# Optimization experiments

Measured on AMD Instinct MI355X. Metric: run time of the kernel, lower is better.

## Reference

```python
import jax, jax.numpy as jnp
import numpy as np

B, L, D_MODEL, N_HEADS = 2, 2048, 1024, 16
HEAD_DIM = D_MODEL // N_HEADS  # 64
PAD_START = (3 * L) // 4  # last quarter of keys are padding


def _rope_tables(seq_len, dim, base=10000.0, dtype=jnp.float32):
    inv_freq = 1.0 / (base ** (jnp.arange(0, dim, 2, dtype=jnp.float32) / dim))
    t = jnp.arange(seq_len, dtype=jnp.float32)
    freqs = jnp.einsum('i,j->ij', t, inv_freq)  # (L, dim/2)
    return jnp.cos(freqs).astype(dtype), jnp.sin(freqs).astype(dtype)


def _apply_rope(x, cos, sin):
    # x: (B, H, L, D); cos/sin: (L, D/2)
    cos = cos[None, None]
    sin = sin[None, None]
    x_even, x_odd = x[..., 0::2], x[..., 1::2]
    rot_even = x_even * cos - x_odd * sin
    rot_odd = x_even * sin + x_odd * cos
    return jnp.stack((rot_even, rot_odd), axis=-1).reshape(x.shape)


def setup_inputs() -> dict:
    key = jax.random.key(0)
    k_x, k_wqkv, k_bqkv, k_wout, k_bout = jax.random.split(key, 5)
    x = jax.random.normal(k_x, (B, L, D_MODEL), dtype=jnp.float32)
    Wqkv = jax.random.normal(k_wqkv, (3 * D_MODEL, D_MODEL), dtype=jnp.float32) * 0.02
    bqkv = jax.random.normal(k_bqkv, (3 * D_MODEL,), dtype=jnp.float32) * 0.02
    Wout = jax.random.normal(k_wout, (D_MODEL, D_MODEL), dtype=jnp.float32) * 0.02
    bout = jax.random.normal(k_bout, (D_MODEL,), dtype=jnp.float32) * 0.02
    # True = padded position (end of sequence padded)
    pad_mask = jnp.broadcast_to(jnp.arange(L) >= PAD_START, (B, L))
    return {"x": x, "pad_mask": pad_mask, "Wqkv": Wqkv, "bqkv": bqkv, "Wout": Wout, "bout": bout}


def reference(x, pad_mask, Wqkv, bqkv, Wout, bout):
    Bc, Lc, E = x.shape
    H, D = N_HEADS, HEAD_DIM
    qkv = x @ Wqkv.T + bqkv                       # (B, L, 3E)
    qkv = qkv.reshape(Bc, Lc, 3, H, D)
    q = jnp.transpose(qkv[:, :, 0], (0, 2, 1, 3))  # (B, H, L, D)
    k = jnp.transpose(qkv[:, :, 1], (0, 2, 1, 3))
    v = jnp.transpose(qkv[:, :, 2], (0, 2, 1, 3))
    cos, sin = _rope_tables(Lc, D, dtype=x.dtype)
    q = _apply_rope(q, cos, sin)
    k = _apply_rope(k, cos, sin)
    # Mask exactly as the torch module builds it: attn_mask = causal_upper | key_pad,
    # with torch bool-mask semantics (True = allowed to attend).
    causal_upper = jnp.triu(jnp.ones((Lc, Lc), dtype=bool), 1)[None, None]  # (1,1,L,L)
    key_pad = pad_mask[:, None, None, :]                                     # (B,1,1,L)
    allowed = causal_upper | key_pad                                         # (B,1,L,L)
    scale = 1.0 / jnp.sqrt(jnp.asarray(D, dtype=x.dtype))
    scores = jnp.einsum('bhqd,bhkd->bhqk', q, k) * scale
    scores = jnp.where(allowed, scores, -jnp.inf)
    attn = jax.nn.softmax(scores, axis=-1)
    out = jnp.einsum('bhqk,bhkd->bhqd', attn, v)   # (B, H, L, D)
    out = jnp.transpose(out, (0, 2, 1, 3)).reshape(Bc, Lc, E)
    return out @ Wout.T + bout
```

## Files before the change

kernel.cpp:

```cpp
#include <hip/hip_runtime.h>

#define BB 2
#define LL 2048
#define DM 1024
#define NH 16
#define HD 64
#define PAD_START 1536

typedef short bf16x8 __attribute__((ext_vector_type(8)));
typedef float f32x4 __attribute__((ext_vector_type(4)));

#define MFMA_B16(a, b, c) __builtin_amdgcn_mfma_f32_16x16x32_bf16(a, b, c, 0, 0, 0)

#define GLOAD_LDS16(g, l)                                            \
    __builtin_amdgcn_global_load_lds(                                \
        (const __attribute__((address_space(1))) void*)(g),          \
        (__attribute__((address_space(3))) void*)(l), 16, 0, 0)

__device__ __forceinline__ float bf2f(unsigned short u) {
    union { unsigned int i; float f; } v; v.i = ((unsigned int)u) << 16; return v.f;
}
__device__ __forceinline__ unsigned short f2bf(float f) {
    union { float f; unsigned int i; } v; v.f = f;
    unsigned int x = v.i;
    return (unsigned short)((x + 0x7fffu + ((x >> 16) & 1u)) >> 16);
}

__global__ __launch_bounds__(256) void split_kernel(
    const float* __restrict__ X, const float* __restrict__ Wq,
    const float* __restrict__ Wo,
    unsigned short* __restrict__ Xh,
    unsigned short* __restrict__ Wh,
    unsigned short* __restrict__ Woh,
    float* __restrict__ cosT, float* __restrict__ sinT)
{
    if (blockIdx.x >= 8192) {
        const int idx = (blockIdx.x - 8192) * 256 + threadIdx.x;
        const int l = idx >> 5, pp = idx & 31;
        const float LOG2_1E4 = 13.287712379549449f;
        const float invf = exp2f(-((float)pp) * (LOG2_1E4 / 32.0f));
        const float ang = (float)l * invf;
        float2 cs; cs.x = cosf(ang); cs.y = sinf(ang);
        ((float2*)cosT)[idx] = cs;
        return;
    }
    const size_t e = ((size_t)blockIdx.x * 256 + threadIdx.x) * 4;
    const float* src; unsigned short* dh; size_t o;
    if (e < 4194304)      { src = X;  dh = Xh;  o = e; }
    else if (e < 7340032) { src = Wq; dh = Wh;  o = e - 4194304; }
    else                  { src = Wo; dh = Woh; o = e - 7340032; }
    float4 v = *(const float4*)(src + o);
    ushort4 hv;
    hv.x = f2bf(v.x); hv.y = f2bf(v.y);
    hv.z = f2bf(v.z); hv.w = f2bf(v.w);
    *(ushort4*)(dh + o) = hv;
}

__device__ __forceinline__ void qk_frag(
    f32x4 cf, int r0, int bh, int d, float bv, float qscale,
    const float2* __restrict__ ct2,
    unsigned short* __restrict__ dst, bool odd)
{
    const int p = d >> 1;
#pragma unroll
    for (int e = 0; e < 4; ++e) {
        const int l = (r0 + e) & (LL - 1);
        const float x = cf[e] + bv;
        const float px = __shfl_xor(x, 1);
        const float2 cs = ct2[l * 32 + p];
        const float ve = odd ? px : x;
        const float vo = odd ? x : px;
        float res = odd ? (ve * cs.y + vo * cs.x) : (ve * cs.x - vo * cs.y);
        res *= qscale;
        const float other = __shfl_xor(res, 1);
        if (!odd) {
            const unsigned int pk = ((unsigned int)f2bf(res)) |
                                    (((unsigned int)f2bf(other)) << 16);
            *(unsigned int*)(dst + ((size_t)bh * LL + l) * HD + d) = pk;
        }
    }
}

__device__ __forceinline__ void v_frag(
    f32x4 cf, int l0, int bh, int d, float bv, unsigned short* __restrict__ vt)
{
    ushort4 pk;
    pk.x = f2bf(cf[0] + bv); pk.y = f2bf(cf[1] + bv);
    pk.z = f2bf(cf[2] + bv); pk.w = f2bf(cf[3] + bv);
    *(ushort4*)(vt + ((size_t)(bh * HD + d)) * LL + l0) = pk;
}

__device__ __forceinline__ void out_frag(
    f32x4 cf, int r0, int c, float bv, float* __restrict__ C)
{
#pragma unroll
    for (int e = 0; e < 4; ++e)
        C[(size_t)(r0 + e) * DM + c] = cf[e] + bv;
}

__global__ __launch_bounds__(512) void qkv_mfma(
    const unsigned short* __restrict__ Xh,
    const unsigned short* __restrict__ Wh,
    const float* __restrict__ bias,
    const float* __restrict__ cosT,
    unsigned short* __restrict__ qs, unsigned short* __restrict__ ks,
    unsigned short* __restrict__ vt)
{
    __shared__ unsigned short As[2 * 256 * 64];
    __shared__ unsigned short Bs[2 * 192 * 64];

    const int bid = blockIdx.y * 16 + blockIdx.x;
    const int xcd = bid & 7;
    const int i   = bid >> 3;
    const int mt  = (xcd & 3) * 4 + (i & 3);
    const int nt  = (xcd >> 2) * 8 + (i >> 2);
    const int m0 = mt * 256, n0 = nt * 192;

    const int t = threadIdx.x;
    const int lane = t & 63;
    const int w = t >> 6;
    const int wm = w >> 2;
    const int wn = w & 3;
    const int lm = lane & 15;
    const int quad = lane >> 4;

    const int rop = lane >> 3;
    const int sw  = ((lane & 7) ^ rop) * 8;
    const unsigned short* ga = Xh + (size_t)(m0 + w * 32 + rop) * 1024 + sw;
    const unsigned short* gb = Wh + (size_t)(n0 + w * 24 + rop) * 1024 + sw;
    unsigned short* lA = As + (w * 32) * 64;
    unsigned short* lB = Bs + (w * 24) * 64;

    const int o1 = (quad ^ (lm & 7)) * 8;
    const int o2 = ((quad + 4) ^ (lm & 7)) * 8;
    const int ar = (wm * 128 + lm) * 64;
    const int br = (wn * 48 + lm) * 64;

    f32x4 acc[8][3];
#pragma unroll
    for (int mf = 0; mf < 8; ++mf)
#pragma unroll
        for (int nf = 0; nf < 3; ++nf) acc[mf][nf] = (f32x4){0.f,0.f,0.f,0.f};

#define STG(ABO, BBO, k0)                                                 \
    do {                                                                  \
        GLOAD_LDS16(ga + (k0),             lA + (ABO));                   \
        GLOAD_LDS16(ga + (k0) +  8 * 1024, lA + (ABO) +  8 * 64);         \
        GLOAD_LDS16(ga + (k0) + 16 * 1024, lA + (ABO) + 16 * 64);         \
        GLOAD_LDS16(ga + (k0) + 24 * 1024, lA + (ABO) + 24 * 64);         \
        GLOAD_LDS16(gb + (k0),             lB + (BBO));                   \
        GLOAD_LDS16(gb + (k0) +  8 * 1024, lB + (BBO) +  8 * 64);         \
        GLOAD_LDS16(gb + (k0) + 16 * 1024, lB + (BBO) + 16 * 64);         \
    } while (0)

#define TILE(ABO, BBO, SG, KS, VMN)                                      \
    {                                                                     \
        bf16x8 af[8][2]; bf16x8 bfr[3][2];                                \
        _Pragma("unroll")                                                 \
        for (int mf = 0; mf < 8; ++mf) {                                  \
            af[mf][0] = *(const bf16x8*)(As + (ABO) + ar + mf * 1024 + o1);\
            af[mf][1] = *(const bf16x8*)(As + (ABO) + ar + mf * 1024 + o2);\
        }                                                                 \
        _Pragma("unroll")                                                 \
        for (int nf = 0; nf < 3; ++nf) {                                  \
            bfr[nf][0] = *(const bf16x8*)(Bs + (BBO) + br + nf * 1024 + o1);\
            bfr[nf][1] = *(const bf16x8*)(Bs + (BBO) + br + nf * 1024 + o2);\
        }                                                                 \
        asm volatile("s_waitcnt lgkmcnt(0)" ::: "memory");                \
        __builtin_amdgcn_sched_barrier(0);                                \
        __builtin_amdgcn_s_barrier();                                     \
        if (SG) { STG(ABO, BBO, KS); }      \
        asm volatile("s_waitcnt vmcnt(" VMN ")" ::: "memory");            \
        __builtin_amdgcn_sched_barrier(0);                                \
        __builtin_amdgcn_s_barrier();                                     \
        __builtin_amdgcn_s_setprio(1);                                    \
        _Pragma("unroll")                                                 \
        for (int mf = 0; mf < 8; ++mf) {                                  \
            _Pragma("unroll")                                             \
            for (int nf = 0; nf < 3; ++nf) {                              \
                acc[mf][nf] = MFMA_B16(af[mf][0], bfr[nf][0], acc[mf][nf]);\
                acc[mf][nf] = MFMA_B16(af[mf][1], bfr[nf][1], acc[mf][nf]);\
            }                                                             \
        }                                                                 \
        __builtin_amdgcn_s_setprio(0);                                    \
    }

    STG(0, 0, 0);
    STG(16384, 12288, 64);
    asm volatile("s_waitcnt vmcnt(7)" ::: "memory");
    __builtin_amdgcn_sched_barrier(0);
    __builtin_amdgcn_s_barrier();

    for (int k0 = 0; k0 < 896; k0 += 128) {
        TILE(0,     0,     1, k0 + 128, "7")
        TILE(16384, 12288, 1, k0 + 192, "7")
    }
    TILE(0,     0,     0, 0, "0")
    TILE(16384, 12288, 0, 0, "0")
#undef TILE
#undef STG

    const int bi = m0 >> 11;
    const int rbase = m0 + wm * 128;
    const int cbase = n0 + wn * 48;
    const bool odd = (lm & 1) != 0;
    const float2* ct2 = (const float2*)cosT;

#pragma unroll
    for (int nf = 0; nf < 3; ++nf) {
        const int col0 = cbase + nf * 16;
        const int s = col0 >> 10;
        const int h = (col0 & 1023) >> 6;
        const int bh = bi * NH + h;
        const int d = (col0 & 63) + lm;
        const float bv = bias[col0 + lm];
        if (s == 2) {
#pragma unroll
            for (int mf = 0; mf < 8; ++mf)
                v_frag(acc[mf][nf], (rbase + mf * 16 + quad * 4) & (LL - 1),
                       bh, d, bv, vt);
        } else {
            unsigned short* dst = (s == 0) ? qs : ks;
            const float qscale = (s == 0) ? 0.125f : 1.0f;
#pragma unroll
            for (int mf = 0; mf < 8; ++mf)
                qk_frag(acc[mf][nf], rbase + mf * 16 + quad * 4, bh,
                        d, bv, qscale, ct2, dst, odd);
        }
    }
}

__global__ __launch_bounds__(256) void attn_mfma(
    const unsigned short* __restrict__ qs,
    const unsigned short* __restrict__ ks,
    const unsigned short* __restrict__ vt,
    unsigned short* __restrict__ aoh)
{
    __shared__ unsigned short Ks[2][64 * 64];
    __shared__ unsigned short Vs[2][64 * 64];
    __shared__ unsigned short Pl[8][16 * 72];

    const int bid = blockIdx.y * 16 + blockIdx.x;
    const int xcd = bid & 7;
    const int j   = bid >> 3;
    const int bh  = xcd * 4 + (j & 3);
    const int qp  = j >> 2;
    const int qtA = qp;
    const int qtB = 31 - qp;
    const int q0A = qtA * 64, q0B = qtB * 64;
    const int b = bh >> 4, h = bh & (NH - 1);
    const int tid = threadIdx.x;
    const int w = tid >> 6;
    const int lane = tid & 63;
    const int lm = lane & 15;
    const int quad = lane >> 4;
    const int qwA = q0A + w * 16;
    const int qwB = q0B + w * 16;

    const unsigned short* qbA = qs + ((size_t)bh * LL + qwA + lm) * HD + quad * 8;
    const unsigned short* qbB = qs + ((size_t)bh * LL + qwB + lm) * HD + quad * 8;
    const bf16x8 qfA0 = *(const bf16x8*)(qbA);
    const bf16x8 qfA1 = *(const bf16x8*)(qbA + 32);
    const bf16x8 qfB0 = *(const bf16x8*)(qbB);
    const bf16x8 qfB1 = *(const bf16x8*)(qbB + 32);

    f32x4 OA[4], OB[4];
#pragma unroll
    for (int dd = 0; dd < 4; ++dd) {
        OA[dd] = (f32x4){0.f, 0.f, 0.f, 0.f};
        OB[dd] = (f32x4){0.f, 0.f, 0.f, 0.f};
    }
    float lrA[4] = {0.f, 0.f, 0.f, 0.f};
    float lrB[4] = {0.f, 0.f, 0.f, 0.f};

    const unsigned short* kbase = ks + (size_t)bh * LL * HD;
    const unsigned short* vtb   = vt + (size_t)bh * HD * LL;
    unsigned short* pwA = &Pl[w][0];
    unsigned short* pwB = &Pl[w + 4][0];

    const int rop = lane >> 3;
    const int sw8 = ((lane & 7) ^ rop) * 8;
    const int r0 = w * 16 + rop;
    const int r1 = w * 16 + 8 + rop;
    const int o1 = (quad ^ (lm & 7)) * 8;
    const int o2 = ((quad + 4) ^ (lm & 7)) * 8;

#define ASTAGE(BUF, KK)                                                      \
    do {                                                                     \
        GLOAD_LDS16(kbase + (size_t)((KK) + r0) * HD + sw8,                  \
                    &Ks[BUF][0] + (w * 2) * 512);                            \
        GLOAD_LDS16(kbase + (size_t)((KK) + r1) * HD + sw8,                  \
                    &Ks[BUF][0] + (w * 2 + 1) * 512);                        \
        GLOAD_LDS16(vtb + (size_t)r0 * LL + (KK) + sw8,                      \
                    &Vs[BUF][0] + (w * 2) * 512);                            \
        GLOAD_LDS16(vtb + (size_t)r1 * LL + (KK) + sw8,                      \
                    &Vs[BUF][0] + (w * 2 + 1) * 512);                        \
    } while (0)

    const int t0A = qtA;
    const int t0B = (qtB < 24) ? qtB : 24;

    ASTAGE(t0A & 1, t0A * 64);
    __syncthreads();

    for (int tt = t0A; tt < 32; ++tt) {
        const int k0 = tt * 64;
        const int cur = tt & 1;
        const unsigned short* Kc = &Ks[cur][0];
        const unsigned short* Vc = &Vs[cur][0];
        const bool doB = (tt >= t0B);

        {
            const int kn = ((tt + 1) < 32 ? (tt + 1) : 31) * 64;
            ASTAGE(cur ^ 1, kn);
        }

        f32x4 sfA[4], sfB[4];
#pragma unroll
        for (int c = 0; c < 4; ++c) {
            const bf16x8 kf0 = *(const bf16x8*)(Kc + (c * 16 + lm) * 64 + o1);
            const bf16x8 kf1 = *(const bf16x8*)(Kc + (c * 16 + lm) * 64 + o2);
            f32x4 zA = (f32x4){0.f, 0.f, 0.f, 0.f};
            zA = MFMA_B16(qfA0, kf0, zA);
            zA = MFMA_B16(qfA1, kf1, zA);
            sfA[c] = zA;
            f32x4 zB = (f32x4){0.f, 0.f, 0.f, 0.f};
            if (doB) {
                zB = MFMA_B16(qfB0, kf0, zB);
                zB = MFMA_B16(qfB1, kf1, zB);
            }
            sfB[c] = zB;
        }
        if (tt == t0A) {
#pragma unroll
            for (int c = 0; c < 4; ++c) {
                const int kg = k0 + c * 16 + lm;
#pragma unroll
                for (int r = 0; r < 4; ++r) {
                    if (kg <= qwA + quad * 4 + r) sfA[c][r] = -1e30f;
                }
            }
        }
        if (doB && tt == t0B && qtB < 24) {
#pragma unroll
            for (int c = 0; c < 4; ++c) {
                const int kg = k0 + c * 16 + lm;
#pragma unroll
                for (int r = 0; r < 4; ++r) {
                    if (kg <= qwB + quad * 4 + r) sfB[c][r] = -1e30f;
                }
            }
        }

#pragma unroll
        for (int r = 0; r < 4; ++r) {
#pragma unroll
            for (int c = 0; c < 4; ++c) {
                const float pA = __expf(sfA[c][r]);
                lrA[r] += pA;
                pwA[(quad * 4 + r) * 72 + c * 16 + lm] = f2bf(pA);
            }
        }
        if (doB) {
#pragma unroll
            for (int r = 0; r < 4; ++r) {
#pragma unroll
                for (int c = 0; c < 4; ++c) {
                    const float pB = __expf(sfB[c][r]);
                    lrB[r] += pB;
                    pwB[(quad * 4 + r) * 72 + c * 16 + lm] = f2bf(pB);
                }
            }
        }

        const bf16x8 aA0 = *(const bf16x8*)(pwA + lm * 72 + quad * 8);
        const bf16x8 aA1 = *(const bf16x8*)(pwA + lm * 72 + 32 + quad * 8);
#pragma unroll
        for (int dd = 0; dd < 4; ++dd) {
            const bf16x8 b0 = *(const bf16x8*)(Vc + (dd * 16 + lm) * 64 + o1);
            const bf16x8 b1 = *(const bf16x8*)(Vc + (dd * 16 + lm) * 64 + o2);
            OA[dd] = MFMA_B16(aA0, b0, OA[dd]);
            OA[dd] = MFMA_B16(aA1, b1, OA[dd]);
        }
        if (doB) {
            const bf16x8 aB0 = *(const bf16x8*)(pwB + lm * 72 + quad * 8);
            const bf16x8 aB1 = *(const bf16x8*)(pwB + lm * 72 + 32 + quad * 8);
#pragma unroll
            for (int dd = 0; dd < 4; ++dd) {
                const bf16x8 b0 = *(const bf16x8*)(Vc + (dd * 16 + lm) * 64 + o1);
                const bf16x8 b1 = *(const bf16x8*)(Vc + (dd * 16 + lm) * 64 + o2);
                OB[dd] = MFMA_B16(aB0, b0, OB[dd]);
                OB[dd] = MFMA_B16(aB1, b1, OB[dd]);
            }
        }

        __syncthreads();
    }
#undef ASTAGE

#pragma unroll
    for (int r = 0; r < 4; ++r) {
        float rsA = lrA[r];
        rsA += __shfl_xor(rsA, 1);
        rsA += __shfl_xor(rsA, 2);
        rsA += __shfl_xor(rsA, 4);
        rsA += __shfl_xor(rsA, 8);
        lrA[r] = rsA;
        float rsB = lrB[r];
        rsB += __shfl_xor(rsB, 1);
        rsB += __shfl_xor(rsB, 2);
        rsB += __shfl_xor(rsB, 4);
        rsB += __shfl_xor(rsB, 8);
        lrB[r] = rsB;
    }

#pragma unroll
    for (int r = 0; r < 4; ++r) {
        const float invA = 1.0f / lrA[r];
        const int qgA = qwA + quad * 4 + r;
        const size_t baseA = ((size_t)(b * LL + qgA)) * DM + h * HD;
#pragma unroll
        for (int dd = 0; dd < 4; ++dd)
            aoh[baseA + dd * 16 + lm] = f2bf(OA[dd][r] * invA);
        const float invB = 1.0f / lrB[r];
        const int qgB = qwB + quad * 4 + r;
        const size_t baseB = ((size_t)(b * LL + qgB)) * DM + h * HD;
#pragma unroll
        for (int dd = 0; dd < 4; ++dd)
            aoh[baseB + dd * 16 + lm] = f2bf(OB[dd][r] * invB);
    }
}

__global__ __launch_bounds__(256) void out_mfma(
    const unsigned short* __restrict__ Ah,
    const unsigned short* __restrict__ Wh,
    const float* __restrict__ bias, float* __restrict__ C)
{
    __shared__ unsigned short As[128 * 64];
    __shared__ unsigned short Bs[128 * 64];
    const int n0 = blockIdx.x * 128;
    const int m0 = blockIdx.y * 128;

    f32x4 c00 = {0,0,0,0}, c01 = {0,0,0,0}, c02 = {0,0,0,0}, c03 = {0,0,0,0};
    f32x4 c10 = {0,0,0,0}, c11 = {0,0,0,0}, c12 = {0,0,0,0}, c13 = {0,0,0,0};
    f32x4 c20 = {0,0,0,0}, c21 = {0,0,0,0}, c22 = {0,0,0,0}, c23 = {0,0,0,0};
    f32x4 c30 = {0,0,0,0}, c31 = {0,0,0,0}, c32 = {0,0,0,0}, c33 = {0,0,0,0};

    const int t = threadIdx.x;
    const int lane = t & 63;
    const int w = t >> 6;
    const int wm = (w >> 1) << 6;
    const int wn = (w & 1) << 6;
    const int lm = lane & 15;
    const int quad = lane >> 4;

    const int rop = lane >> 3;
    const int sw  = ((lane & 7) ^ rop) * 8;
    const unsigned short* ga = Ah + (size_t)(m0 + w * 32 + rop) * 1024 + sw;
    const unsigned short* gb = Wh + (size_t)(n0 + w * 32 + rop) * 1024 + sw;
    unsigned short* lA = As + (w * 32) * 64;
    unsigned short* lB = Bs + (w * 32) * 64;

    const int o1 = (quad ^ (lm & 7)) * 8;
    const int o2 = ((quad + 4) ^ (lm & 7)) * 8;
    const int arow = (wm + lm) * 64;
    const int brow = (wn + lm) * 64;

    for (int k0 = 0; k0 < 1024; k0 += 64) {
        __syncthreads();
        GLOAD_LDS16(ga + k0,             lA);
        GLOAD_LDS16(ga + k0 +  8 * 1024, lA +  8 * 64);
        GLOAD_LDS16(ga + k0 + 16 * 1024, lA + 16 * 64);
        GLOAD_LDS16(ga + k0 + 24 * 1024, lA + 24 * 64);
        GLOAD_LDS16(gb + k0,             lB);
        GLOAD_LDS16(gb + k0 +  8 * 1024, lB +  8 * 64);
        GLOAD_LDS16(gb + k0 + 16 * 1024, lB + 16 * 64);
        GLOAD_LDS16(gb + k0 + 24 * 1024, lB + 24 * 64);
        __syncthreads();
        {
            bf16x8 a0 = *(const bf16x8*)(As + arow +  0 * 64 + o1);
            bf16x8 a1 = *(const bf16x8*)(As + arow + 16 * 64 + o1);
            bf16x8 a2 = *(const bf16x8*)(As + arow + 32 * 64 + o1);
            bf16x8 a3 = *(const bf16x8*)(As + arow + 48 * 64 + o1);
            bf16x8 b0 = *(const bf16x8*)(Bs + brow +  0 * 64 + o1);
            bf16x8 b1 = *(const bf16x8*)(Bs + brow + 16 * 64 + o1);
            bf16x8 b2 = *(const bf16x8*)(Bs + brow + 32 * 64 + o1);
            bf16x8 b3 = *(const bf16x8*)(Bs + brow + 48 * 64 + o1);
            c00 = MFMA_B16(a0, b0, c00); c01 = MFMA_B16(a0, b1, c01);
            c02 = MFMA_B16(a0, b2, c02); c03 = MFMA_B16(a0, b3, c03);
            c10 = MFMA_B16(a1, b0, c10); c11 = MFMA_B16(a1, b1, c11);
            c12 = MFMA_B16(a1, b2, c12); c13 = MFMA_B16(a1, b3, c13);
            c20 = MFMA_B16(a2, b0, c20); c21 = MFMA_B16(a2, b1, c21);
            c22 = MFMA_B16(a2, b2, c22); c23 = MFMA_B16(a2, b3, c23);
            c30 = MFMA_B16(a3, b0, c30); c31 = MFMA_B16(a3, b1, c31);
            c32 = MFMA_B16(a3, b2, c32); c33 = MFMA_B16(a3, b3, c33);
        }
        {
            bf16x8 a0 = *(const bf16x8*)(As + arow +  0 * 64 + o2);
            bf16x8 a1 = *(const bf16x8*)(As + arow + 16 * 64 + o2);
            bf16x8 a2 = *(const bf16x8*)(As + arow + 32 * 64 + o2);
            bf16x8 a3 = *(const bf16x8*)(As + arow + 48 * 64 + o2);
            bf16x8 b0 = *(const bf16x8*)(Bs + brow +  0 * 64 + o2);
            bf16x8 b1 = *(const bf16x8*)(Bs + brow + 16 * 64 + o2);
            bf16x8 b2 = *(const bf16x8*)(Bs + brow + 32 * 64 + o2);
            bf16x8 b3 = *(const bf16x8*)(Bs + brow + 48 * 64 + o2);
            c00 = MFMA_B16(a0, b0, c00); c01 = MFMA_B16(a0, b1, c01);
            c02 = MFMA_B16(a0, b2, c02); c03 = MFMA_B16(a0, b3, c03);
            c10 = MFMA_B16(a1, b0, c10); c11 = MFMA_B16(a1, b1, c11);
            c12 = MFMA_B16(a1, b2, c12); c13 = MFMA_B16(a1, b3, c13);
            c20 = MFMA_B16(a2, b0, c20); c21 = MFMA_B16(a2, b1, c21);
            c22 = MFMA_B16(a2, b2, c22); c23 = MFMA_B16(a2, b3, c23);
            c30 = MFMA_B16(a3, b0, c30); c31 = MFMA_B16(a3, b1, c31);
            c32 = MFMA_B16(a3, b2, c32); c33 = MFMA_B16(a3, b3, c33);
        }
    }

#define CSTORE(rt, ct) \
    out_frag(c##rt##ct, m0 + wm + rt * 16 + quad * 4, \
             n0 + wn + ct * 16 + lm, bias[n0 + wn + ct * 16 + lm], C);
    CSTORE(0,0) CSTORE(0,1) CSTORE(0,2) CSTORE(0,3)
    CSTORE(1,0) CSTORE(1,1) CSTORE(1,2) CSTORE(1,3)
    CSTORE(2,0) CSTORE(2,1) CSTORE(2,2) CSTORE(2,3)
    CSTORE(3,0) CSTORE(3,1) CSTORE(3,2) CSTORE(3,3)
#undef CSTORE
}

extern "C" void kernel_launch(void* const* d_in, const int* in_sizes, int n_in,
                              void* d_out, int out_size, void* d_ws, size_t ws_size,
                              hipStream_t stream)
{
    const float* x    = (const float*)d_in[0];
    const float* Wqkv = (const float*)d_in[2];
    const float* bqkv = (const float*)d_in[3];
    const float* Wout = (const float*)d_in[4];
    const float* bout = (const float*)d_in[5];
    float* out = (float*)d_out;

    unsigned short* p = (unsigned short*)d_ws;
    const size_t SZ = (size_t)BB * NH * LL * HD;
    unsigned short* qsb = p; p += SZ;
    unsigned short* ksb = p; p += SZ;
    unsigned short* vtb = p; p += SZ;
    unsigned short* Xhi = p; p += SZ;
    unsigned short* Whi = p; p += (size_t)3145728;
    unsigned short* Wohi = p; p += (size_t)1048576;
    float* cosT = (float*)p; p += (size_t)4 * 65536;

    split_kernel<<<8448, 256, 0, stream>>>(x, Wqkv, Wout,
                                           Xhi, Whi, Wohi, cosT, nullptr);
    dim3 g1(16, 16);
    qkv_mfma<<<g1, 512, 0, stream>>>(Xhi, Whi, bqkv, cosT,
                                     qsb, ksb, vtb);
    dim3 g2(16, 32);
    attn_mfma<<<g2, 256, 0, stream>>>(qsb, ksb, vtb, Xhi);
    dim3 g3(8, 32);
    out_mfma<<<g3, 256, 0, stream>>>(Xhi, Wohi, bout, out);
}
```

Measured before the change: 200.1 us.

## Double-buffer out-projection GEMM, simplify RoPE epilogue, drop sched barriers and setprio

The output-projection GEMM now uses two LDS buffers, so the next 64-wide K slice is loaded while the current one feeds the MFMAs. This removes the load-then-compute serialisation and one barrier per step, at the cost of twice the LDS. The QKV RoPE epilogue now lets even lanes compute both rotated outputs directly, which removes one shuffle and the odd-lane cos/sin load. The sched_barrier and setprio hints in the QKV GEMM main loop are also removed, which hands instruction ordering back to the compiler.

```diff
diff --git a/kernel.cpp b/kernel.cpp
--- a/kernel.cpp
+++ b/kernel.cpp
@@ -59,23 +59,20 @@
 __device__ __forceinline__ void qk_frag(
     f32x4 cf, int r0, int bh, int d, float bv, float qscale,
     const float2* __restrict__ ct2,
-    unsigned short* __restrict__ dst, bool odd)
+    unsigned short* __restrict__ dst, bool even)
 {
     const int p = d >> 1;
 #pragma unroll
     for (int e = 0; e < 4; ++e) {
         const int l = (r0 + e) & (LL - 1);
         const float x = cf[e] + bv;
-        const float px = __shfl_xor(x, 1);
-        const float2 cs = ct2[l * 32 + p];
-        const float ve = odd ? px : x;
-        const float vo = odd ? x : px;
-        float res = odd ? (ve * cs.y + vo * cs.x) : (ve * cs.x - vo * cs.y);
-        res *= qscale;
-        const float other = __shfl_xor(res, 1);
-        if (!odd) {
-            const unsigned int pk = ((unsigned int)f2bf(res)) |
-                                    (((unsigned int)f2bf(other)) << 16);
+        const float xo = __shfl_xor(x, 1);
+        if (even) {
+            const float2 cs = ct2[l * 32 + p];
+            const float re = (x * cs.x - xo * cs.y) * qscale;
+            const float ro = (x * cs.y + xo * cs.x) * qscale;
+            const unsigned int pk = ((unsigned int)f2bf(re)) |
+                                    (((unsigned int)f2bf(ro)) << 16);
             *(unsigned int*)(dst + ((size_t)bh * LL + l) * HD + d) = pk;
         }
     }
@@ -167,13 +164,10 @@
             bfr[nf][1] = *(const bf16x8*)(Bs + (BBO) + br + nf * 1024 + o2);\
         }                                                                 \
         asm volatile("s_waitcnt lgkmcnt(0)" ::: "memory");                \
-        __builtin_amdgcn_sched_barrier(0);                                \
         __builtin_amdgcn_s_barrier();                                     \
         if (SG) { STG(ABO, BBO, KS); }      \
         asm volatile("s_waitcnt vmcnt(" VMN ")" ::: "memory");            \
-        __builtin_amdgcn_sched_barrier(0);                                \
         __builtin_amdgcn_s_barrier();                                     \
-        __builtin_amdgcn_s_setprio(1);                                    \
         _Pragma("unroll")                                                 \
         for (int mf = 0; mf < 8; ++mf) {                                  \
             _Pragma("unroll")                                             \
@@ -182,13 +176,11 @@
                 acc[mf][nf] = MFMA_B16(af[mf][1], bfr[nf][1], acc[mf][nf]);\
             }                                                             \
         }                                                                 \
-        __builtin_amdgcn_s_setprio(0);                                    \
     }
 
     STG(0, 0, 0);
     STG(16384, 12288, 64);
     asm volatile("s_waitcnt vmcnt(7)" ::: "memory");
-    __builtin_amdgcn_sched_barrier(0);
     __builtin_amdgcn_s_barrier();
 
     for (int k0 = 0; k0 < 896; k0 += 128) {
@@ -203,7 +195,7 @@
     const int bi = m0 >> 11;
     const int rbase = m0 + wm * 128;
     const int cbase = n0 + wn * 48;
-    const bool odd = (lm & 1) != 0;
+    const bool even = (lm & 1) == 0;
     const float2* ct2 = (const float2*)cosT;
 
 #pragma unroll
@@ -225,7 +217,7 @@
 #pragma unroll
             for (int mf = 0; mf < 8; ++mf)
                 qk_frag(acc[mf][nf], rbase + mf * 16 + quad * 4, bh,
-                        d, bv, qscale, ct2, dst, odd);
+                        d, bv, qscale, ct2, dst, even);
         }
     }
 }
@@ -436,8 +428,8 @@
     const unsigned short* __restrict__ Wh,
     const float* __restrict__ bias, float* __restrict__ C)
 {
-    __shared__ unsigned short As[128 * 64];
-    __shared__ unsigned short Bs[128 * 64];
+    __shared__ unsigned short As[2 * 128 * 64];
+    __shared__ unsigned short Bs[2 * 128 * 64];
     const int n0 = blockIdx.x * 128;
     const int m0 = blockIdx.y * 128;
 
@@ -466,54 +458,53 @@
     const int arow = (wm + lm) * 64;
     const int brow = (wn + lm) * 64;
 
-    for (int k0 = 0; k0 < 1024; k0 += 64) {
+#define STAGE64(bufofs, k0)                                               \
+    do {                                                                  \
+        GLOAD_LDS16(ga + (k0),             lA + (bufofs));                \
+        GLOAD_LDS16(ga + (k0) +  8 * 1024, lA + (bufofs) +  8 * 64);      \
+        GLOAD_LDS16(ga + (k0) + 16 * 1024, lA + (bufofs) + 16 * 64);      \
+        GLOAD_LDS16(ga + (k0) + 24 * 1024, lA + (bufofs) + 24 * 64);      \
+        GLOAD_LDS16(gb + (k0),             lB + (bufofs));                \
+        GLOAD_LDS16(gb + (k0) +  8 * 1024, lB + (bufofs) +  8 * 64);      \
+        GLOAD_LDS16(gb + (k0) + 16 * 1024, lB + (bufofs) + 16 * 64);      \
+        GLOAD_LDS16(gb + (k0) + 24 * 1024, lB + (bufofs) + 24 * 64);      \
+    } while (0)
+
+#define GEMM_HALF(as_, bs_, oo)                                           \
+    do {                                                                  \
+        bf16x8 a0 = *(const bf16x8*)((as_) + arow +  0 * 64 + (oo));      \
+        bf16x8 a1 = *(const bf16x8*)((as_) + arow + 16 * 64 + (oo));      \
+        bf16x8 a2 = *(const bf16x8*)((as_) + arow + 32 * 64 + (oo));      \
+        bf16x8 a3 = *(const bf16x8*)((as_) + arow + 48 * 64 + (oo));      \
+        bf16x8 b0 = *(const bf16x8*)((bs_) + brow +  0 * 64 + (oo));      \
+        bf16x8 b1 = *(const bf16x8*)((bs_) + brow + 16 * 64 + (oo));      \
+        bf16x8 b2 = *(const bf16x8*)((bs_) + brow + 32 * 64 + (oo));      \
+        bf16x8 b3 = *(const bf16x8*)((bs_) + brow + 48 * 64 + (oo));      \
+        c00 = MFMA_B16(a0, b0, c00); c01 = MFMA_B16(a0, b1, c01);         \
+        c02 = MFMA_B16(a0, b2, c02); c03 = MFMA_B16(a0, b3, c03);         \
+        c10 = MFMA_B16(a1, b0, c10); c11 = MFMA_B16(a1, b1, c11);         \
+        c12 = MFMA_B16(a1, b2, c12); c13 = MFMA_B16(a1, b3, c13);         \
+        c20 = MFMA_B16(a2, b0, c20); c21 = MFMA_B16(a2, b1, c21);         \
+        c22 = MFMA_B16(a2, b2, c22); c23 = MFMA_B16(a2, b3, c23);         \
+        c30 = MFMA_B16(a3, b0, c30); c31 = MFMA_B16(a3, b1, c31);         \
+        c32 = MFMA_B16(a3, b2, c32); c33 = MFMA_B16(a3, b3, c33);         \
+    } while (0)
+
+    STAGE64(0, 0);
+    __syncthreads();
+
+    for (int k0 = 0; k0 < 1024; k0 += 128) {
+        STAGE64(8192, k0 + 64);
+        GEMM_HALF(As, Bs, o1);
+        GEMM_HALF(As, Bs, o2);
         __syncthreads();
-        GLOAD_LDS16(ga + k0,             lA);
-        GLOAD_LDS16(ga + k0 +  8 * 1024, lA +  8 * 64);
-        GLOAD_LDS16(ga + k0 + 16 * 1024, lA + 16 * 64);
-        GLOAD_LDS16(ga + k0 + 24 * 1024, lA + 24 * 64);
-        GLOAD_LDS16(gb + k0,             lB);
-        GLOAD_LDS16(gb + k0 +  8 * 1024, lB +  8 * 64);
-        GLOAD_LDS16(gb + k0 + 16 * 1024, lB + 16 * 64);
-        GLOAD_LDS16(gb + k0 + 24 * 1024, lB + 24 * 64);
+        if (k0 + 128 < 1024) STAGE64(0, k0 + 128);
+        GEMM_HALF(As + 8192, Bs + 8192, o1);
+        GEMM_HALF(As + 8192, Bs + 8192, o2);
         __syncthreads();
-        {
-            bf16x8 a0 = *(const bf16x8*)(As + arow +  0 * 64 + o1);
-            bf16x8 a1 = *(const bf16x8*)(As + arow + 16 * 64 + o1);
-            bf16x8 a2 = *(const bf16x8*)(As + arow + 32 * 64 + o1);
-            bf16x8 a3 = *(const bf16x8*)(As + arow + 48 * 64 + o1);
-            bf16x8 b0 = *(const bf16x8*)(Bs + brow +  0 * 64 + o1);
-            bf16x8 b1 = *(const bf16x8*)(Bs + brow + 16 * 64 + o1);
-            bf16x8 b2 = *(const bf16x8*)(Bs + brow + 32 * 64 + o1);
-            bf16x8 b3 = *(const bf16x8*)(Bs + brow + 48 * 64 + o1);
-            c00 = MFMA_B16(a0, b0, c00); c01 = MFMA_B16(a0, b1, c01);
-            c02 = MFMA_B16(a0, b2, c02); c03 = MFMA_B16(a0, b3, c03);
-            c10 = MFMA_B16(a1, b0, c10); c11 = MFMA_B16(a1, b1, c11);
-            c12 = MFMA_B16(a1, b2, c12); c13 = MFMA_B16(a1, b3, c13);
-            c20 = MFMA_B16(a2, b0, c20); c21 = MFMA_B16(a2, b1, c21);
-            c22 = MFMA_B16(a2, b2, c22); c23 = MFMA_B16(a2, b3, c23);
-            c30 = MFMA_B16(a3, b0, c30); c31 = MFMA_B16(a3, b1, c31);
-            c32 = MFMA_B16(a3, b2, c32); c33 = MFMA_B16(a3, b3, c33);
-        }
-        {
-            bf16x8 a0 = *(const bf16x8*)(As + arow +  0 * 64 + o2);
-            bf16x8 a1 = *(const bf16x8*)(As + arow + 16 * 64 + o2);
-            bf16x8 a2 = *(const bf16x8*)(As + arow + 32 * 64 + o2);
-            bf16x8 a3 = *(const bf16x8*)(As + arow + 48 * 64 + o2);
-            bf16x8 b0 = *(const bf16x8*)(Bs + brow +  0 * 64 + o2);
-            bf16x8 b1 = *(const bf16x8*)(Bs + brow + 16 * 64 + o2);
-            bf16x8 b2 = *(const bf16x8*)(Bs + brow + 32 * 64 + o2);
-            bf16x8 b3 = *(const bf16x8*)(Bs + brow + 48 * 64 + o2);
-            c00 = MFMA_B16(a0, b0, c00); c01 = MFMA_B16(a0, b1, c01);
-            c02 = MFMA_B16(a0, b2, c02); c03 = MFMA_B16(a0, b3, c03);
-            c10 = MFMA_B16(a1, b0, c10); c11 = MFMA_B16(a1, b1, c11);
-            c12 = MFMA_B16(a1, b2, c12); c13 = MFMA_B16(a1, b3, c13);
-            c20 = MFMA_B16(a2, b0, c20); c21 = MFMA_B16(a2, b1, c21);
-            c22 = MFMA_B16(a2, b2, c22); c23 = MFMA_B16(a2, b3, c23);
-            c30 = MFMA_B16(a3, b0, c30); c31 = MFMA_B16(a3, b1, c31);
-            c32 = MFMA_B16(a3, b2, c32); c33 = MFMA_B16(a3, b3, c33);
-        }
-    }
+    }
+#undef STAGE64
+#undef GEMM_HALF
 
 #define CSTORE(rt, ct) \
     out_frag(c##rt##ct, m0 + wm + rt * 16 + quad * 4, \
```

New measurement: 205.1 us. 2.5% more time.
